# Kernel optimization log

Measured on AMD Instinct MI355X. Metric: run time of the kernel, lower is better.

The kernel has to match this reference:

```python
import jax, jax.numpy as jnp
import numpy as np

IN_DIM = 128
D_MODEL = 2 * IN_DIM        # 256, Mamba d_model
D_INNER = 2 * D_MODEL       # 512, expand=2
D_STATE = 16
D_CONV = 4
DT_RANK = (D_MODEL + 15) // 16  # 16
B = 4
C = 1024                    # original channel dim -> Mamba sequence length
EPS = 1e-5


def rmsnorm(x, w):
    return x * jax.lax.rsqrt(jnp.mean(x * x, axis=-1, keepdims=True) + EPS) * w


def conv1x1(x, w, b):
    # x: (B, Cin, L); 1x1 conv == channel matmul
    return jnp.einsum('oi,bil->bol', w, x) + b[None, :, None]


def mamba(u, in_w, conv_w, conv_b, xproj_w, dt_w, dt_b, A_log, Dp, out_w):
    # u: (B, L, D_MODEL) -- faithful mamba_ssm Mamba block (defaults)
    di, K = conv_w.shape
    n = A_log.shape[1]
    r = dt_w.shape[1]
    xz = u @ in_w.T                              # (B,L,2*di)
    xx, z = jnp.split(xz, 2, axis=-1)
    # depthwise causal conv over L
    xt = jnp.pad(jnp.transpose(xx, (0, 2, 1)), ((0, 0), (0, 0), (K - 1, 0)))
    xc = jax.lax.conv_general_dilated(xt, conv_w[:, None, :], (1,), 'VALID',
                                      feature_group_count=di)
    xx = jax.nn.silu(jnp.transpose(xc + conv_b[None, :, None], (0, 2, 1)))
    dbl = xx @ xproj_w.T                         # (B,L,r+2n)
    dt, Bm, Cm = dbl[..., :r], dbl[..., r:r + n], dbl[..., r + n:]
    dt = jax.nn.softplus(dt @ dt_w.T + dt_b)     # (B,L,di)
    A = -jnp.exp(A_log)                          # (di,n)
    dA = jnp.exp(dt[..., None] * A)              # (B,L,di,n)
    dBx = (dt * xx)[..., None] * Bm[:, :, None, :]

    def step(h, inps):
        dA_t, dBx_t, C_t = inps
        h = dA_t * h + dBx_t
        return h, jnp.einsum('bdn,bn->bd', h, C_t)

    h0 = jnp.zeros((u.shape[0], di, n), u.dtype)
    _, ys = jax.lax.scan(step, h0, (jnp.moveaxis(dA, 1, 0),
                                    jnp.moveaxis(dBx, 1, 0),
                                    jnp.moveaxis(Cm, 1, 0)))
    y = jnp.moveaxis(ys, 0, 1) + xx * Dp
    return (y * jax.nn.silu(z)) @ out_w.T


def postnorm_mamba(u, params, norm_w):
    return rmsnorm(mamba(u, *params), norm_w) + u


def _forward(x, W_in, b_in, W_wp, b_wp, W_fp, b_fp, W_bp, b_bp, W_out, b_out,
             norm_w_top,
             f_in_w, f_conv_w, f_conv_b, f_xproj_w, f_dt_w, f_dt_b, f_A_log, f_D, f_out_w, f_norm_w,
             bk_in_w, bk_conv_w, bk_conv_b, bk_xproj_w, bk_dt_w, bk_dt_b, bk_A_log, bk_D, bk_out_w, bk_norm_w):
    residual = x                                  # (B, C, L)
    xn = rmsnorm(x, norm_w_top)                   # RMSNorm over L
    xt = jnp.transpose(xn, (0, 2, 1))             # (B, L, C); L acts as conv channels
    ssm_in = conv1x1(xt, W_in, b_in)              # (B, 2L, C)
    # forward branch
    fwd = conv1x1(ssm_in, W_fp, b_fp)
    fwd = jnp.transpose(fwd, (0, 2, 1))           # (B, C, 2L): Mamba seq=C
    fwd = postnorm_mamba(fwd, (f_in_w, f_conv_w, f_conv_b, f_xproj_w, f_dt_w,
                               f_dt_b, f_A_log, f_D, f_out_w), f_norm_w)
    fwd = jnp.transpose(fwd, (0, 2, 1))           # (B, 2L, C)
    # backward branch (flip along C)
    bwd = conv1x1(ssm_in[:, :, ::-1], W_bp, b_bp)
    bwd = jnp.transpose(bwd, (0, 2, 1))
    bwd = postnorm_mamba(bwd, (bk_in_w, bk_conv_w, bk_conv_b, bk_xproj_w, bk_dt_w,
                               bk_dt_b, bk_A_log, bk_D, bk_out_w), bk_norm_w)
    bwd = jnp.transpose(bwd, (0, 2, 1))[:, :, ::-1]
    # swish gate
    w = conv1x1(xt, W_wp, b_wp)
    w = w * jax.nn.sigmoid(w)
    out = conv1x1(w * fwd + w * bwd, W_out, b_out)  # (B, L, C)
    return jnp.transpose(out, (0, 2, 1)) + residual  # (B, C, L)


def setup_inputs():
    key = jax.random.key(0)
    ks = iter(jax.random.split(key, 64))
    rn = lambda shape, s=0.02: jax.random.normal(next(ks), shape, jnp.float32) * s
    inp = {"x": jax.random.normal(next(ks), (B, C, IN_DIM), jnp.float32)}
    inp["W_in"] = rn((2 * IN_DIM, IN_DIM));   inp["b_in"] = rn((2 * IN_DIM,), 0.1)
    inp["W_wp"] = rn((2 * IN_DIM, IN_DIM));   inp["b_wp"] = rn((2 * IN_DIM,), 0.1)
    inp["W_fp"] = rn((2 * IN_DIM, 2 * IN_DIM)); inp["b_fp"] = rn((2 * IN_DIM,), 0.1)
    inp["W_bp"] = rn((2 * IN_DIM, 2 * IN_DIM)); inp["b_bp"] = rn((2 * IN_DIM,), 0.1)
    inp["W_out"] = rn((IN_DIM, 2 * IN_DIM));  inp["b_out"] = rn((IN_DIM,), 0.1)
    inp["norm_w_top"] = jnp.ones((IN_DIM,), jnp.float32)
    A_init = jnp.log(jnp.broadcast_to(jnp.arange(1, D_STATE + 1, dtype=jnp.float32),
                                      (D_INNER, D_STATE)))
    for p in ("f", "bk"):
        inp[p + "_in_w"] = rn((2 * D_INNER, D_MODEL))
        inp[p + "_conv_w"] = rn((D_INNER, D_CONV), 0.2)
        inp[p + "_conv_b"] = rn((D_INNER,), 0.1)
        inp[p + "_xproj_w"] = rn((DT_RANK + 2 * D_STATE, D_INNER))
        inp[p + "_dt_w"] = rn((D_INNER, DT_RANK), 0.1)
        inp[p + "_dt_b"] = rn((D_INNER,), 0.5)
        inp[p + "_A_log"] = A_init
        inp[p + "_D"] = jnp.ones((D_INNER,), jnp.float32)
        inp[p + "_out_w"] = rn((D_MODEL, D_INNER))
        inp[p + "_norm_w"] = jnp.ones((D_MODEL,), jnp.float32)
    return inp


def reference(x, W_in, b_in, W_wp, b_wp, W_fp, b_fp, W_bp, b_bp, W_out, b_out,
              norm_w_top,
              f_in_w, f_conv_w, f_conv_b, f_xproj_w, f_dt_w, f_dt_b, f_A_log, f_D, f_out_w, f_norm_w,
              bk_in_w, bk_conv_w, bk_conv_b, bk_xproj_w, bk_dt_w, bk_dt_b, bk_A_log, bk_D, bk_out_w, bk_norm_w):
    return _forward(x, W_in, b_in, W_wp, b_wp, W_fp, b_fp, W_bp, b_bp, W_out, b_out,
                    norm_w_top,
                    f_in_w, f_conv_w, f_conv_b, f_xproj_w, f_dt_w, f_dt_b, f_A_log, f_D, f_out_w, f_norm_w,
                    bk_in_w, bk_conv_w, bk_conv_b, bk_xproj_w, bk_dt_w, bk_dt_b, bk_A_log, bk_D, bk_out_w, bk_norm_w)
```

## Files before the change

kernel.cpp:

```cpp
#include <hip/hip_runtime.h>
#include <math.h>

#define C_LEN 1024
#define NROW 4096
#define NCHUNK 32
#define CHUNK 32

typedef __attribute__((ext_vector_type(8))) short short8;
typedef __attribute__((ext_vector_type(4))) float f32x4;

__device__ __forceinline__ float siluf(float x) { return x / (1.f + __expf(-x)); }

__device__ __forceinline__ unsigned short f2bf(float f) {
    unsigned u = __builtin_bit_cast(unsigned, f);
    unsigned r = (u + 0x7FFFu + ((u >> 16) & 1u)) >> 16;
    return (unsigned short)r;
}
__device__ __forceinline__ float bf2f(unsigned short v) {
    unsigned u = ((unsigned)v) << 16;
    return __builtin_bit_cast(float, u);
}

struct WTab {
    const float* s[6];
    unsigned short* d[6];
    int n[6];
};
__global__ __launch_bounds__(256) void k_prep(WTab t, const float* __restrict__ x,
                                              const float* __restrict__ nw,
                                              unsigned short* __restrict__ xn_bf,
                                              const float* __restrict__ W_fp,
                                              const float* __restrict__ W_bp,
                                              const float* __restrict__ W_in,
                                              const float* __restrict__ b_in,
                                              const float* __restrict__ b_fp,
                                              const float* __restrict__ b_bp,
                                              const float* __restrict__ b_wp,
                                              float* __restrict__ Wpin,
                                              float* __restrict__ bmega,
                                              unsigned short* __restrict__ Wmega) {
    int seg = blockIdx.y;
    if (seg < 6) {
        int n = t.n[seg];
        int i = (blockIdx.x * 256 + threadIdx.x) * 4;
        if (i < n) {
            float4 v = *(const float4*)(t.s[seg] + i);
            unsigned short* o = t.d[seg] + i;
            o[0] = f2bf(v.x); o[1] = f2bf(v.y); o[2] = f2bf(v.z); o[3] = f2bf(v.w);
        }
    } else if (seg == 6) {
        int wave = threadIdx.x >> 6, lane = threadIdx.x & 63;
        #pragma unroll
        for (int it = 0; it < 4; ++it) {
            int row = blockIdx.x * 16 + it * 4 + wave;
            if (row < 4096) {
                float2 v = ((const float2*)(x + (size_t)row * 128))[lane];
                float ss = v.x * v.x + v.y * v.y;
                #pragma unroll
                for (int off = 32; off; off >>= 1) ss += __shfl_xor(ss, off, 64);
                float rs = rsqrtf(ss * (1.f / 128.f) + 1e-5f);
                float2 wv = ((const float2*)nw)[lane];
                ushort2 o;
                o.x = f2bf(v.x * rs * wv.x);
                o.y = f2bf(v.y * rs * wv.y);
                ((ushort2*)(xn_bf + (size_t)row * 128))[lane] = o;
            }
        }
    } else {
        int tg = blockIdx.x * 256 + threadIdx.x;
        if (tg < 65536) {
            int p = tg >> 15, rem = tg & 32767;
            int o = rem >> 7, i = rem & 127;
            const float* Wsrc = p ? W_bp : W_fp;
            float s = 0.f;
            #pragma unroll 8
            for (int j = 0; j < 256; ++j) s += Wsrc[o * 256 + j] * W_in[j * 128 + i];
            Wpin[p * 32768 + o * 128 + i] = s;
            Wmega[(size_t)(p * 256 + o) * 128 + i] = f2bf(s);
        } else if (tg < 66048) {
            int q = tg - 65536;
            int p = q >> 8, o = q & 255;
            const float* Wsrc = p ? W_bp : W_fp;
            const float* badd = p ? b_bp : b_fp;
            float s = badd[o];
            #pragma unroll 8
            for (int j = 0; j < 256; ++j) s += Wsrc[o * 256 + j] * b_in[j];
            bmega[p * 256 + o] = s;
        } else if (tg < 66304) {
            int q = tg - 66048;
            bmega[512 + q] = b_wp[q];
        }
    }
}

__global__ __launch_bounds__(256) void k_wcomb2(const float* __restrict__ f_in_w,
                                                const float* __restrict__ bk_in_w,
                                                const float* __restrict__ Wpin,
                                                unsigned short* __restrict__ Wmega,
                                                float* __restrict__ bmega) {
    int tg = blockIdx.x * 256 + threadIdx.x;
    if (tg < 262144) {
        int p = tg >> 17, rem = tg & 131071;
        int o = rem >> 7, i = rem & 127;
        const float* inw = p ? bk_in_w : f_in_w;
        const float* wp = Wpin + p * 32768;
        float s = 0.f;
        #pragma unroll 8
        for (int j = 0; j < 256; ++j) s += inw[o * 256 + j] * wp[j * 128 + i];
        Wmega[(size_t)(768 + p * 1024 + o) * 128 + i] = f2bf(s);
    } else if (tg < 264192) {
        int q = tg - 262144;
        int p = q >> 10, o = q & 1023;
        const float* inw = p ? bk_in_w : f_in_w;
        const float* bp = bmega + p * 256;
        float s = 0.f;
        #pragma unroll 8
        for (int j = 0; j < 256; ++j) s += inw[o * 256 + j] * bp[j];
        bmega[768 + p * 1024 + o] = s;
    }
}

__global__ __launch_bounds__(256) void k_megagemm(const unsigned short* __restrict__ A,
                                                  const unsigned short* __restrict__ W,
                                                  const float* __restrict__ bias,
                                                  unsigned short* __restrict__ uf,
                                                  unsigned short* __restrict__ ub,
                                                  unsigned short* __restrict__ wbuf,
                                                  unsigned short* __restrict__ xzF,
                                                  unsigned short* __restrict__ xzB) {
    __shared__ __align__(16) unsigned short As[128 * 72];
    __shared__ __align__(16) unsigned short Bs[64 * 72];
    const int K = 128;
    int tid = threadIdx.x;
    int m0 = blockIdx.y * 128, n0 = blockIdx.x * 64;
    int w = tid >> 6, lane = tid & 63;
    int q = lane >> 4, ln = lane & 15;

    unsigned short* Cb; int stride, nc0; bool flip = false, dosilu = false;
    if (n0 < 256)       { Cb = uf;   stride = 256;  nc0 = n0; }
    else if (n0 < 512)  { Cb = ub;   stride = 256;  nc0 = n0 - 256;  flip = true; }
    else if (n0 < 768)  { Cb = wbuf; stride = 256;  nc0 = n0 - 512;  dosilu = true; }
    else if (n0 < 1792) { Cb = xzF;  stride = 1024; nc0 = n0 - 768; }
    else                { Cb = xzB;  stride = 1024; nc0 = n0 - 1792; flip = true; }

    int arow0 = tid >> 1;
    int aseg0 = (tid & 1) * 32;
    int brow = tid >> 2, bseg = (tid & 3) * 16;
    const unsigned short* pa = A + (size_t)(m0 + arow0) * K + aseg0;
    const unsigned short* pw = W + (size_t)(n0 + brow) * K + bseg;

    f32x4 acc[2][4];
    #pragma unroll
    for (int i = 0; i < 2; ++i)
        #pragma unroll
        for (int j = 0; j < 4; ++j) acc[i][j] = (f32x4)(0.f);

    for (int k0 = 0; k0 < K; k0 += 64) {
        #pragma unroll
        for (int h = 0; h < 4; ++h)
            *(short8*)&As[arow0 * 72 + aseg0 + h * 8] = *(const short8*)(pa + h * 8);
        *(short8*)&Bs[brow * 72 + bseg]     = *(const short8*)pw;
        *(short8*)&Bs[brow * 72 + bseg + 8] = *(const short8*)(pw + 8);
        pa += 64; pw += 64;
        __syncthreads();
        short8 a0[2], a1[2];
        #pragma unroll
        for (int i = 0; i < 2; ++i) {
            int row = w * 32 + i * 16 + ln;
            a0[i] = *(const short8*)&As[row * 72 + q * 8];
            a1[i] = *(const short8*)&As[row * 72 + 32 + q * 8];
        }
        #pragma unroll
        for (int j = 0; j < 4; ++j) {
            short8 bf0 = *(const short8*)&Bs[(j * 16 + ln) * 72 + q * 8];
            short8 bf1 = *(const short8*)&Bs[(j * 16 + ln) * 72 + 32 + q * 8];
            #pragma unroll
            for (int i = 0; i < 2; ++i) {
                acc[i][j] = __builtin_amdgcn_mfma_f32_16x16x32_bf16(a0[i], bf0, acc[i][j], 0, 0, 0);
                acc[i][j] = __builtin_amdgcn_mfma_f32_16x16x32_bf16(a1[i], bf1, acc[i][j], 0, 0, 0);
            }
        }
        __syncthreads();
    }
    #pragma unroll
    for (int j = 0; j < 4; ++j) {
        float bsv = bias[n0 + j * 16 + ln];
        int nc = nc0 + j * 16 + ln;
        #pragma unroll
        for (int i = 0; i < 2; ++i) {
            #pragma unroll
            for (int r = 0; r < 4; ++r) {
                int m = m0 + w * 32 + i * 16 + q * 4 + r;
                int mw = flip ? (m ^ (C_LEN - 1)) : m;
                float v = acc[i][j][r] + bsv;
                if (dosilu) v = siluf(v);
                Cb[(size_t)mw * stride + nc] = f2bf(v);
            }
        }
    }
}

__global__ __launch_bounds__(256) void k_gemm128(
        const unsigned short* __restrict__ A0, const unsigned short* __restrict__ A1,
        const unsigned short* __restrict__ W0, const unsigned short* __restrict__ W1,
        unsigned short* __restrict__ Cb0, unsigned short* __restrict__ Cb1,
        int N, int K) {
    __shared__ __align__(16) unsigned short As[128 * 72];
    __shared__ __align__(16) unsigned short Bs[64 * 72];
    int p = blockIdx.z;
    const unsigned short* A = p ? A1 : A0;
    const unsigned short* W = p ? W1 : W0;
    unsigned short* Cbf = p ? Cb1 : Cb0;
    int tid = threadIdx.x;
    int m0 = blockIdx.y * 128, n0 = blockIdx.x * 64;
    int w = tid >> 6, lane = tid & 63;
    int q = lane >> 4, ln = lane & 15;

    int arow0 = tid >> 1;
    int aseg0 = (tid & 1) * 32;
    int brow = tid >> 2, bseg = (tid & 3) * 16;
    const unsigned short* pa = A + (size_t)(m0 + arow0) * K + aseg0;
    const unsigned short* pw = W + (size_t)(n0 + brow) * K + bseg;

    f32x4 acc[2][4];
    #pragma unroll
    for (int i = 0; i < 2; ++i)
        #pragma unroll
        for (int j = 0; j < 4; ++j) acc[i][j] = (f32x4)(0.f);

    for (int k0 = 0; k0 < K; k0 += 64) {
        #pragma unroll
        for (int h = 0; h < 4; ++h)
            *(short8*)&As[arow0 * 72 + aseg0 + h * 8] = *(const short8*)(pa + h * 8);
        *(short8*)&Bs[brow * 72 + bseg]     = *(const short8*)pw;
        *(short8*)&Bs[brow * 72 + bseg + 8] = *(const short8*)(pw + 8);
        pa += 64; pw += 64;
        __syncthreads();
        short8 a0[2], a1[2];
        #pragma unroll
        for (int i = 0; i < 2; ++i) {
            int row = w * 32 + i * 16 + ln;
            a0[i] = *(const short8*)&As[row * 72 + q * 8];
            a1[i] = *(const short8*)&As[row * 72 + 32 + q * 8];
        }
        #pragma unroll
        for (int j = 0; j < 4; ++j) {
            short8 bf0 = *(const short8*)&Bs[(j * 16 + ln) * 72 + q * 8];
            short8 bf1 = *(const short8*)&Bs[(j * 16 + ln) * 72 + 32 + q * 8];
            #pragma unroll
            for (int i = 0; i < 2; ++i) {
                acc[i][j] = __builtin_amdgcn_mfma_f32_16x16x32_bf16(a0[i], bf0, acc[i][j], 0, 0, 0);
                acc[i][j] = __builtin_amdgcn_mfma_f32_16x16x32_bf16(a1[i], bf1, acc[i][j], 0, 0, 0);
            }
        }
        __syncthreads();
    }
    #pragma unroll
    for (int i = 0; i < 2; ++i)
        #pragma unroll
        for (int j = 0; j < 4; ++j) {
            int nn = n0 + j * 16 + ln;
            #pragma unroll
            for (int r = 0; r < 4; ++r) {
                int m = m0 + w * 32 + i * 16 + q * 4 + r;
                Cbf[(size_t)m * N + nn] = f2bf(acc[i][j][r]);
            }
        }
}

__global__ __launch_bounds__(256) void k_gemm2f(
        const unsigned short* __restrict__ A0, const unsigned short* __restrict__ A1,
        const unsigned short* __restrict__ W0, const unsigned short* __restrict__ W1,
        float* __restrict__ Cf0, float* __restrict__ Cf1,
        int N, int K) {
    __shared__ __align__(16) unsigned short As[64 * 72];
    __shared__ __align__(16) unsigned short Bs[64 * 72];
    int p = blockIdx.z;
    const unsigned short* A = p ? A1 : A0;
    const unsigned short* W = p ? W1 : W0;
    float* Cf = p ? Cf1 : Cf0;
    int tid = threadIdx.x;
    int m0 = blockIdx.y * 64, n0 = blockIdx.x * 64;
    int w = tid >> 6, lane = tid & 63;
    int q = lane >> 4, ln = lane & 15;
    int srow = tid >> 2;
    int sseg = (tid & 3) * 16;

    const unsigned short* pa = A + (size_t)(m0 + srow) * K + sseg;
    int nIdx = n0 + srow;
    const unsigned short* pw = W + (size_t)nIdx * K + sseg;
    bool nOK = (nIdx < N);

    f32x4 acc[4];
    #pragma unroll
    for (int j = 0; j < 4; ++j) acc[j] = (f32x4)(0.f);

    for (int k0 = 0; k0 < K; k0 += 64) {
        *(short8*)&As[srow * 72 + sseg]     = *(const short8*)pa;
        *(short8*)&As[srow * 72 + sseg + 8] = *(const short8*)(pa + 8);
        short8 b0 = (short8)(0), b1 = (short8)(0);
        if (nOK) { b0 = *(const short8*)pw; b1 = *(const short8*)(pw + 8); }
        *(short8*)&Bs[srow * 72 + sseg] = b0;
        *(short8*)&Bs[srow * 72 + sseg + 8] = b1;
        pa += 64; pw += 64;
        __syncthreads();
        short8 af0 = *(const short8*)&As[(w * 16 + ln) * 72 + q * 8];
        short8 af1 = *(const short8*)&As[(w * 16 + ln) * 72 + 32 + q * 8];
        #pragma unroll
        for (int j = 0; j < 4; ++j) {
            short8 bf0 = *(const short8*)&Bs[(j * 16 + ln) * 72 + q * 8];
            short8 bf1 = *(const short8*)&Bs[(j * 16 + ln) * 72 + 32 + q * 8];
            acc[j] = __builtin_amdgcn_mfma_f32_16x16x32_bf16(af0, bf0, acc[j], 0, 0, 0);
            acc[j] = __builtin_amdgcn_mfma_f32_16x16x32_bf16(af1, bf1, acc[j], 0, 0, 0);
        }
        __syncthreads();
    }
    #pragma unroll
    for (int j = 0; j < 4; ++j) {
        int nn = n0 + j * 16 + ln;
        if (nn < N) {
            #pragma unroll
            for (int r = 0; r < 4; ++r) {
                int m = m0 + w * 16 + q * 4 + r;
                Cf[(size_t)m * N + nn] = acc[j][r];
            }
        }
    }
}

__global__ __launch_bounds__(256) void k_gemm_out(const unsigned short* __restrict__ A,
                                                  const unsigned short* __restrict__ W,
                                                  const float* __restrict__ bias,
                                                  const float* __restrict__ resid,
                                                  float* __restrict__ Cf) {
    __shared__ __align__(16) unsigned short As[64 * 72];
    __shared__ __align__(16) unsigned short Bs[64 * 72];
    const int N = 128, K = 256;
    int tid = threadIdx.x;
    int m0 = blockIdx.y * 64, n0 = blockIdx.x * 64;
    int w = tid >> 6, lane = tid & 63;
    int q = lane >> 4, ln = lane & 15;
    int srow = tid >> 2;
    int sseg = (tid & 3) * 16;

    const unsigned short* pa = A + (size_t)(m0 + srow) * K + sseg;
    const unsigned short* pw = W + (size_t)(n0 + srow) * K + sseg;

    f32x4 acc[4];
    #pragma unroll
    for (int j = 0; j < 4; ++j) acc[j] = (f32x4)(0.f);

    for (int k0 = 0; k0 < K; k0 += 64) {
        *(short8*)&As[srow * 72 + sseg]     = *(const short8*)pa;
        *(short8*)&As[srow * 72 + sseg + 8] = *(const short8*)(pa + 8);
        *(short8*)&Bs[srow * 72 + sseg]     = *(const short8*)pw;
        *(short8*)&Bs[srow * 72 + sseg + 8] = *(const short8*)(pw + 8);
        pa += 64; pw += 64;
        __syncthreads();
        short8 af0 = *(const short8*)&As[(w * 16 + ln) * 72 + q * 8];
        short8 af1 = *(const short8*)&As[(w * 16 + ln) * 72 + 32 + q * 8];
        #pragma unroll
        for (int j = 0; j < 4; ++j) {
            short8 bf0 = *(const short8*)&Bs[(j * 16 + ln) * 72 + q * 8];
            short8 bf1 = *(const short8*)&Bs[(j * 16 + ln) * 72 + 32 + q * 8];
            acc[j] = __builtin_amdgcn_mfma_f32_16x16x32_bf16(af0, bf0, acc[j], 0, 0, 0);
            acc[j] = __builtin_amdgcn_mfma_f32_16x16x32_bf16(af1, bf1, acc[j], 0, 0, 0);
        }
        __syncthreads();
    }
    #pragma unroll
    for (int j = 0; j < 4; ++j) {
        int nn = n0 + j * 16 + ln;
        float bsv = bias[nn];
        #pragma unroll
        for (int r = 0; r < 4; ++r) {
            int m = m0 + w * 16 + q * 4 + r;
            Cf[(size_t)m * N + nn] = acc[j][r] + bsv + resid[(size_t)m * N + nn];
        }
    }
}

__global__ __launch_bounds__(256) void k_conv(const unsigned short* __restrict__ xz0,
                                              const unsigned short* __restrict__ xz1,
                                              const float* __restrict__ cw0,
                                              const float* __restrict__ cw1,
                                              const float* __restrict__ cb0,
                                              const float* __restrict__ cb1,
                                              unsigned short* __restrict__ xc0,
                                              unsigned short* __restrict__ xc1) {
    int pz = blockIdx.z;
    const unsigned short* xz = pz ? xz1 : xz0;
    const float* cw = pz ? cw1 : cw0;
    const float* cb = pz ? cb1 : cb0;
    unsigned short* xconv_bf = pz ? xc1 : xc0;
    int d = blockIdx.x * 256 + threadIdx.x;
    int by = blockIdx.y;
    int b = by >> 6, c0 = (by & 63) * 16;
    float4 cwv = *(const float4*)(cw + d * 4);
    float bias = cb[d];
    const unsigned short* base = xz + (size_t)(b * C_LEN) * 1024 + d;
    float w0 = 0.f, w1 = 0.f, w2 = 0.f;
    if (c0) {
        w0 = bf2f(base[(size_t)(c0 - 3) * 1024]);
        w1 = bf2f(base[(size_t)(c0 - 2) * 1024]);
        w2 = bf2f(base[(size_t)(c0 - 1) * 1024]);
    }
    unsigned short* out = xconv_bf + (size_t)(b * C_LEN + c0) * 512 + d;
    #pragma unroll
    for (int i = 0; i < 16; ++i) {
        float cur = bf2f(base[(size_t)(c0 + i) * 1024]);
        float acc = bias;
        acc = fmaf(cwv.x, w0, acc);
        acc = fmaf(cwv.y, w1, acc);
        acc = fmaf(cwv.z, w2, acc);
        acc = fmaf(cwv.w, cur, acc);
        out[(size_t)i * 512] = f2bf(siluf(acc));
        w0 = w1; w1 = w2; w2 = cur;
    }
}

__global__ __launch_bounds__(256) void k_dtproj(const float* __restrict__ dbl0,
                                                const float* __restrict__ dbl1,
                                                const float* __restrict__ dtw0,
                                                const float* __restrict__ dtw1,
                                                const float* __restrict__ dtb0,
                                                const float* __restrict__ dtb1,
                                                unsigned short* __restrict__ dt0,
                                                unsigned short* __restrict__ dt1) {
    int pz = blockIdx.z;
    const float* dbl = pz ? dbl1 : dbl0;
    const float* dtw = pz ? dtw1 : dtw0;
    const float* dtb = pz ? dtb1 : dtb0;
    unsigned short* dt = pz ? dt1 : dt0;
    int d = blockIdx.x * 256 + threadIdx.x;
    int r0 = blockIdx.y * 8;
    float4 w0 = *(const float4*)(dtw + d * 16);
    float4 w1 = *(const float4*)(dtw + d * 16 + 4);
    float4 w2 = *(const float4*)(dtw + d * 16 + 8);
    float4 w3 = *(const float4*)(dtw + d * 16 + 12);
    float bias = dtb[d];
    #pragma unroll
    for (int rr = 0; rr < 8; ++rr) {
        int r = r0 + rr;
        const float* row = dbl + (size_t)r * 48;
        float s = bias;
        s = fmaf(row[0], w0.x, s);  s = fmaf(row[1], w0.y, s);
        s = fmaf(row[2], w0.z, s);  s = fmaf(row[3], w0.w, s);
        s = fmaf(row[4], w1.x, s);  s = fmaf(row[5], w1.y, s);
        s = fmaf(row[6], w1.z, s);  s = fmaf(row[7], w1.w, s);
        s = fmaf(row[8], w2.x, s);  s = fmaf(row[9], w2.y, s);
        s = fmaf(row[10], w2.z, s); s = fmaf(row[11], w2.w, s);
        s = fmaf(row[12], w3.x, s); s = fmaf(row[13], w3.y, s);
        s = fmaf(row[14], w3.z, s); s = fmaf(row[15], w3.w, s);
        float sp = fmaxf(s, 0.f) + log1pf(__expf(-fabsf(s)));
        dt[(size_t)r * 512 + d] = f2bf(sp);
    }
}

__global__ __launch_bounds__(256) void k_scan1(const unsigned short* __restrict__ dt0,
                                               const unsigned short* __restrict__ dt1,
                                               const unsigned short* __restrict__ xc0,
                                               const unsigned short* __restrict__ xc1,
                                               const float* __restrict__ dblA,
                                               const float* __restrict__ dblB,
                                               const float* __restrict__ alog0,
                                               const float* __restrict__ alog1,
                                               float* __restrict__ hfin0,
                                               float* __restrict__ hfin1,
                                               float* __restrict__ Pfin0,
                                               float* __restrict__ Pfin1) {
    int z = blockIdx.z;
    int b = z & 3, p = z >> 2;
    const unsigned short* dt = p ? dt1 : dt0;
    const unsigned short* xconv_bf = p ? xc1 : xc0;
    const float* dbl = p ? dblB : dblA;
    const float* A_log = p ? alog1 : alog0;
    float* hfin = p ? hfin1 : hfin0;
    float* Pfin = p ? Pfin1 : Pfin0;
    int tid = threadIdx.x;
    int nh = tid & 1, dl = tid >> 1;
    int k = blockIdx.x, dg = blockIdx.y;
    int d = dg * 128 + dl;
    float4 al0 = *(const float4*)&A_log[d * 16 + nh * 8];
    float4 al1 = *(const float4*)&A_log[d * 16 + nh * 8 + 4];
    float Ac[8] = {-__expf(al0.x), -__expf(al0.y), -__expf(al0.z), -__expf(al0.w),
                   -__expf(al1.x), -__expf(al1.y), -__expf(al1.z), -__expf(al1.w)};
    size_t r0 = (size_t)(b * C_LEN + k * CHUNK);
    const unsigned short* pdt = dt + r0 * 512 + d;
    const unsigned short* pxv = xconv_bf + r0 * 512 + d;
    const float* pB  = dbl + r0 * 48 + 16 + nh * 8;
    float h[8] = {0.f, 0.f, 0.f, 0.f, 0.f, 0.f, 0.f, 0.f};
    float sdt = 0.f;
    #pragma unroll 8
    for (int c = 0; c < CHUNK; ++c) {
        float dtv = bf2f(*pdt);
        float xv  = bf2f(*pxv);
        float4 B0 = *(const float4*)pB;
        float4 B1 = *(const float4*)(pB + 4);
        float dx = dtv * xv;
        float Bv[8] = {B0.x, B0.y, B0.z, B0.w, B1.x, B1.y, B1.z, B1.w};
        #pragma unroll
        for (int j = 0; j < 8; ++j)
            h[j] = fmaf(__expf(dtv * Ac[j]), h[j], dx * Bv[j]);
        sdt += dtv;
        pdt += 512; pxv += 512; pB += 48;
    }
    size_t idx = ((size_t)(b * NCHUNK + k) * 512 + d) * 16 + nh * 8;
    *(float4*)&hfin[idx]     = make_float4(h[0], h[1], h[2], h[3]);
    *(float4*)&hfin[idx + 4] = make_float4(h[4], h[5], h[6], h[7]);
    *(float4*)&Pfin[idx]     = make_float4(__expf(Ac[0] * sdt), __expf(Ac[1] * sdt),
                                           __expf(Ac[2] * sdt), __expf(Ac[3] * sdt));
    *(float4*)&Pfin[idx + 4] = make_float4(__expf(Ac[4] * sdt), __expf(Ac[5] * sdt),
                                           __expf(Ac[6] * sdt), __expf(Ac[7] * sdt));
}

__global__ __launch_bounds__(256) void k_scan2(const float* __restrict__ hfin0,
                                               const float* __restrict__ hfin1,
                                               float* __restrict__ Pfin0,
                                               float* __restrict__ Pfin1) {
    int tt = blockIdx.x * 256 + threadIdx.x;
    int p = tt >> 15;
    int t = tt & 32767;
    const float* hfin = p ? hfin1 : hfin0;
    float* Pfin = p ? Pfin1 : Pfin0;
    int b = t >> 13;
    int dn = t & 8191;
    float carry = 0.f;
    #pragma unroll
    for (int k = 0; k < NCHUNK; ++k) {
        size_t idx = (size_t)(b * NCHUNK + k) * 8192 + dn;
        float pv = Pfin[idx];
        float hf = hfin[idx];
        Pfin[idx] = carry;
        carry = fmaf(pv, carry, hf);
    }
}

__global__ __launch_bounds__(256) void k_scan3(const unsigned short* __restrict__ dt0,
                                               const unsigned short* __restrict__ dt1,
                                               const unsigned short* __restrict__ xc0,
                                               const unsigned short* __restrict__ xc1,
                                               const float* __restrict__ dblA,
                                               const float* __restrict__ dblB,
                                               const unsigned short* __restrict__ xz0,
                                               const unsigned short* __restrict__ xz1,
                                               const float* __restrict__ alog0,
                                               const float* __restrict__ alog1,
                                               const float* __restrict__ Dp0,
                                               const float* __restrict__ Dp1,
                                               const float* __restrict__ carry0,
                                               const float* __restrict__ carry1,
                                               unsigned short* __restrict__ g0,
                                               unsigned short* __restrict__ g1) {
    int z = blockIdx.z;
    int b = z & 3, p = z >> 2;
    const unsigned short* dt = p ? dt1 : dt0;
    const unsigned short* xconv_bf = p ? xc1 : xc0;
    const float* dbl = p ? dblB : dblA;
    const unsigned short* xz = p ? xz1 : xz0;
    const float* A_log = p ? alog1 : alog0;
    const float* Dp = p ? Dp1 : Dp0;
    const float* carryArr = p ? carry1 : carry0;
    unsigned short* gated_bf = p ? g1 : g0;
    int tid = threadIdx.x;
    int nh = tid & 1, dl = tid >> 1;
    int k = blockIdx.x, dg = blockIdx.y;
    int d = dg * 128 + dl;
    float4 al0 = *(const float4*)&A_log[d * 16 + nh * 8];
    float4 al1 = *(const float4*)&A_log[d * 16 + nh * 8 + 4];
    float Ac[8] = {-__expf(al0.x), -__expf(al0.y), -__expf(al0.z), -__expf(al0.w),
                   -__expf(al1.x), -__expf(al1.y), -__expf(al1.z), -__expf(al1.w)};
    float Dd = Dp[d];
    size_t idx = ((size_t)(b * NCHUNK + k) * 512 + d) * 16 + nh * 8;
    float4 h0 = *(const float4*)&carryArr[idx];
    float4 h1 = *(const float4*)&carryArr[idx + 4];
    float h[8] = {h0.x, h0.y, h0.z, h0.w, h1.x, h1.y, h1.z, h1.w};
    size_t r0 = (size_t)(b * C_LEN + k * CHUNK);
    const unsigned short* pdt = dt + r0 * 512 + d;
    const unsigned short* pxv = xconv_bf + r0 * 512 + d;
    const float* pB  = dbl + r0 * 48 + 16 + nh * 8;
    const float* pC  = dbl + r0 * 48 + 32 + nh * 8;
    const unsigned short* pz = xz + r0 * 1024 + 512 + d;
    unsigned short* pg = gated_bf + r0 * 512 + d;
    #pragma unroll 4
    for (int c = 0; c < CHUNK; ++c) {
        float dtv = bf2f(*pdt);
        float xv  = bf2f(*pxv);
        float4 B0 = *(const float4*)pB;
        float4 B1 = *(const float4*)(pB + 4);
        float4 C0 = *(const float4*)pC;
        float4 C1 = *(const float4*)(pC + 4);
        float dx = dtv * xv;
        float Bv[8] = {B0.x, B0.y, B0.z, B0.w, B1.x, B1.y, B1.z, B1.w};
        float Cv[8] = {C0.x, C0.y, C0.z, C0.w, C1.x, C1.y, C1.z, C1.w};
        float contrib = 0.f;
        #pragma unroll
        for (int j = 0; j < 8; ++j) {
            h[j] = fmaf(__expf(dtv * Ac[j]), h[j], dx * Bv[j]);
            contrib = fmaf(h[j], Cv[j], contrib);
        }
        contrib += __shfl_xor(contrib, 1, 64);
        if (nh == 0) {
            float y = contrib + xv * Dd;
            float zv = bf2f(*pz);
            *pg = f2bf(y * siluf(zv));
        }
        pdt += 512; pxv += 512; pB += 48; pC += 48; pz += 1024; pg += 512;
    }
}

__global__ __launch_bounds__(256) void k_postcomb(const unsigned short* __restrict__ mo0,
                                                  const unsigned short* __restrict__ mo1,
                                                  const float* __restrict__ w0,
                                                  const float* __restrict__ w1,
                                                  const unsigned short* __restrict__ uf,
                                                  const unsigned short* __restrict__ ub,
                                                  const unsigned short* __restrict__ wbuf,
                                                  unsigned short* __restrict__ Acomb) {
    __shared__ float red[8];
    int r = blockIdx.x, t = threadIdx.x;
    int rf = r ^ (C_LEN - 1);
    float v0 = bf2f(mo0[(size_t)r * 256 + t]);
    float v1 = bf2f(mo1[(size_t)rf * 256 + t]);
    float ss0 = v0 * v0, ss1 = v1 * v1;
    #pragma unroll
    for (int off = 32; off; off >>= 1) {
        ss0 += __shfl_xor(ss0, off, 64);
        ss1 += __shfl_xor(ss1, off, 64);
    }
    if ((t & 63) == 0) { red[t >> 6] = ss0; red[4 + (t >> 6)] = ss1; }
    __syncthreads();
    float rs0 = rsqrtf((red[0] + red[1] + red[2] + red[3]) * (1.f / 256.f) + 1e-5f);
    float rs1 = rsqrtf((red[4] + red[5] + red[6] + red[7]) * (1.f / 256.f) + 1e-5f);
    float mofv = v0 * rs0 * w0[t] + bf2f(uf[(size_t)r * 256 + t]);
    float mobv = v1 * rs1 * w1[t] + bf2f(ub[(size_t)rf * 256 + t]);
    Acomb[(size_t)r * 256 + t] = f2bf(bf2f(wbuf[(size_t)r * 256 + t]) * (mofv + mobv));
}

extern "C" void kernel_launch(void* const* d_in, const int* in_sizes, int n_in,
                              void* d_out, int out_size, void* d_ws, size_t ws_size,
                              hipStream_t stream) {
    const float* x          = (const float*)d_in[0];
    const float* W_in       = (const float*)d_in[1];
    const float* b_in       = (const float*)d_in[2];
    const float* W_wp       = (const float*)d_in[3];
    const float* b_wp       = (const float*)d_in[4];
    const float* W_fp       = (const float*)d_in[5];
    const float* b_fp       = (const float*)d_in[6];
    const float* W_bp       = (const float*)d_in[7];
    const float* b_bp       = (const float*)d_in[8];
    const float* W_out      = (const float*)d_in[9];
    const float* b_out      = (const float*)d_in[10];
    const float* norm_w_top = (const float*)d_in[11];
    const float* mamba_p[2][10];
    for (int p = 0; p < 2; ++p)
        for (int i = 0; i < 10; ++i)
            mamba_p[p][i] = (const float*)d_in[12 + p * 10 + i];

    float* ws = (float*)d_ws;
    float* dblP[2]  = {ws + 0,       ws + 196608};
    unsigned short* dtsP[2] = {(unsigned short*)(ws + 393216),
                               (unsigned short*)(ws + 2490368)};
    float* Wpin  = ws + 1441792;
    float* bmega = ws + 1507328;
    float* hfinP[2] = {ws + 4587520, ws + 5636096};
    float* PfinP[2] = {ws + 6684672, ws + 7733248};

    unsigned short* us = (unsigned short*)(ws + 8781824);
    unsigned short* xn_bf   = us + 0;
    unsigned short* Acomb   = us + 524288;
    unsigned short* uf_bf   = us + 1572864;
    unsigned short* ub_bf   = us + 2621440;
    unsigned short* wbuf_bf = us + 3670016;
    unsigned short* xzP[2]  = {us + 4718592,  us + 8912896};
    unsigned short* xcP[2]  = {us + 13107200, us + 15204352};
    unsigned short* gP[2]   = {us + 17301504, us + 19398656};
    unsigned short* moP[2]  = {us + 21495808, us + 22544384};
    unsigned short* Wmega   = us + 23592960;
    unsigned short* wb      = us + 25690112;
    unsigned short* wb_W_out = wb + 196608;
    unsigned short* wb_xp[2]  = {wb + 491520, wb + 909312};
    unsigned short* wb_outw[2]= {wb + 516096, wb + 933888};

    WTab t;
    t.s[0] = W_wp;            t.d[0] = Wmega + 512 * 128; t.n[0] = 32768;
    t.s[1] = W_out;           t.d[1] = wb_W_out;          t.n[1] = 32768;
    t.s[2] = mamba_p[0][3];   t.d[2] = wb_xp[0];          t.n[2] = 24576;
    t.s[3] = mamba_p[0][8];   t.d[3] = wb_outw[0];        t.n[3] = 131072;
    t.s[4] = mamba_p[1][3];   t.d[4] = wb_xp[1];          t.n[4] = 24576;
    t.s[5] = mamba_p[1][8];   t.d[5] = wb_outw[1];        t.n[5] = 131072;
    k_prep<<<dim3(260, 8), 256, 0, stream>>>(t, x, norm_w_top, xn_bf,
                                             W_fp, W_bp, W_in, b_in, b_fp, b_bp, b_wp,
                                             Wpin, bmega, Wmega);
    k_wcomb2<<<1040, 256, 0, stream>>>(mamba_p[0][0], mamba_p[1][0], Wpin, Wmega, bmega);
    k_megagemm<<<dim3(44, 32), 256, 0, stream>>>(xn_bf, Wmega, bmega,
                                                 uf_bf, ub_bf, wbuf_bf, xzP[0], xzP[1]);
    k_conv<<<dim3(2, 256, 2), 256, 0, stream>>>(xzP[0], xzP[1],
                                                mamba_p[0][1], mamba_p[1][1],
                                                mamba_p[0][2], mamba_p[1][2],
                                                xcP[0], xcP[1]);
    k_gemm2f<<<dim3(1, 64, 2), 256, 0, stream>>>(xcP[0], xcP[1], wb_xp[0], wb_xp[1],
                                                 dblP[0], dblP[1], 48, 512);
    k_dtproj<<<dim3(2, 512, 2), 256, 0, stream>>>(dblP[0], dblP[1],
                                                  mamba_p[0][4], mamba_p[1][4],
                                                  mamba_p[0][5], mamba_p[1][5],
                                                  dtsP[0], dtsP[1]);
    k_scan1<<<dim3(NCHUNK, 4, 8), 256, 0, stream>>>(dtsP[0], dtsP[1], xcP[0], xcP[1],
                                                    dblP[0], dblP[1],
                                                    mamba_p[0][6], mamba_p[1][6],
                                                    hfinP[0], hfinP[1], PfinP[0], PfinP[1]);
    k_scan2<<<256, 256, 0, stream>>>(hfinP[0], hfinP[1], PfinP[0], PfinP[1]);
    k_scan3<<<dim3(NCHUNK, 4, 8), 256, 0, stream>>>(dtsP[0], dtsP[1], xcP[0], xcP[1],
                                                    dblP[0], dblP[1], xzP[0], xzP[1],
                                                    mamba_p[0][6], mamba_p[1][6],
                                                    mamba_p[0][7], mamba_p[1][7],
                                                    PfinP[0], PfinP[1], gP[0], gP[1]);
    k_gemm128<<<dim3(4, 32, 2), 256, 0, stream>>>(gP[0], gP[1], wb_outw[0], wb_outw[1],
                                                  moP[0], moP[1], 256, 512);
    k_postcomb<<<NROW, 256, 0, stream>>>(moP[0], moP[1],
                                         mamba_p[0][9], mamba_p[1][9],
                                         uf_bf, ub_bf, wbuf_bf, Acomb);
    k_gemm_out<<<dim3(2, 64), 256, 0, stream>>>(Acomb, wb_W_out, b_out, x, (float*)d_out);
}
```

Before: 278.3 us.

## Fuse conv, x-projection and dt-projection; fuse post-norm combine into output GEMM

New measurement: 372.9 us. 34.0% more time.

```diff
diff --git a/kernel.cpp b/kernel.cpp
--- a/kernel.cpp
+++ b/kernel.cpp
@@ -268,44 +268,87 @@
         }
 }
 
-__global__ __launch_bounds__(256) void k_gemm2f(
-        const unsigned short* __restrict__ A0, const unsigned short* __restrict__ A1,
+__global__ __launch_bounds__(256) void k_convdbl(
+        const unsigned short* __restrict__ xz0, const unsigned short* __restrict__ xz1,
+        const float* __restrict__ cw0, const float* __restrict__ cw1,
+        const float* __restrict__ cb0, const float* __restrict__ cb1,
         const unsigned short* __restrict__ W0, const unsigned short* __restrict__ W1,
+        const float* __restrict__ dtw0, const float* __restrict__ dtw1,
+        const float* __restrict__ dtb0, const float* __restrict__ dtb1,
+        unsigned short* __restrict__ xcO0, unsigned short* __restrict__ xcO1,
         float* __restrict__ Cf0, float* __restrict__ Cf1,
-        int N, int K) {
-    __shared__ __align__(16) unsigned short As[64 * 72];
+        unsigned short* __restrict__ dtO0, unsigned short* __restrict__ dtO1) {
+    __shared__ __align__(16) unsigned short As64[64 * 520];
     __shared__ __align__(16) unsigned short Bs[64 * 72];
-    int p = blockIdx.z;
-    const unsigned short* A = p ? A1 : A0;
+    __shared__ float dblS[64][17];
+    const int N = 48, K = 512;
+    int p = blockIdx.y;
+    const unsigned short* xz = p ? xz1 : xz0;
+    const float* cw = p ? cw1 : cw0;
+    const float* cb = p ? cb1 : cb0;
     const unsigned short* W = p ? W1 : W0;
+    const float* dtw = p ? dtw1 : dtw0;
+    const float* dtb = p ? dtb1 : dtb0;
+    unsigned short* xcO = p ? xcO1 : xcO0;
     float* Cf = p ? Cf1 : Cf0;
+    unsigned short* dtO = p ? dtO1 : dtO0;
+
     int tid = threadIdx.x;
-    int m0 = blockIdx.y * 64, n0 = blockIdx.x * 64;
+    int m0 = blockIdx.x * 64;
+    int bstart = m0 & ~(C_LEN - 1);
+
+    {
+        int d0 = tid * 2;
+        float4 cwa = *(const float4*)(cw + d0 * 4);
+        float4 cwb = *(const float4*)(cw + d0 * 4 + 4);
+        float cba = cb[d0], cbb = cb[d0 + 1];
+        float a0 = 0.f, a1 = 0.f, a2 = 0.f;
+        float b0 = 0.f, b1 = 0.f, b2 = 0.f;
+        for (int r = m0 - 3; r < m0 + 64; ++r) {
+            float ca = 0.f, cbv = 0.f;
+            if (r >= bstart) {
+                unsigned u = *(const unsigned*)(xz + (size_t)r * 1024 + d0);
+                ca  = bf2f((unsigned short)(u & 0xFFFFu));
+                cbv = bf2f((unsigned short)(u >> 16));
+            }
+            if (r >= m0) {
+                float sa = cba, sb = cbb;
+                sa = fmaf(cwa.x, a0, sa); sa = fmaf(cwa.y, a1, sa);
+                sa = fmaf(cwa.z, a2, sa); sa = fmaf(cwa.w, ca, sa);
+                sb = fmaf(cwb.x, b0, sb); sb = fmaf(cwb.y, b1, sb);
+                sb = fmaf(cwb.z, b2, sb); sb = fmaf(cwb.w, cbv, sb);
+                unsigned short oa = f2bf(siluf(sa));
+                unsigned short ob = f2bf(siluf(sb));
+                unsigned pack = (unsigned)oa | ((unsigned)ob << 16);
+                *(unsigned*)&As64[(r - m0) * 520 + d0] = pack;
+                *(unsigned*)(xcO + (size_t)r * 512 + d0) = pack;
+            }
+            a0 = a1; a1 = a2; a2 = ca;
+            b0 = b1; b1 = b2; b2 = cbv;
+        }
+    }
+    __syncthreads();
+
     int w = tid >> 6, lane = tid & 63;
     int q = lane >> 4, ln = lane & 15;
     int srow = tid >> 2;
     int sseg = (tid & 3) * 16;
-
-    const unsigned short* pa = A + (size_t)(m0 + srow) * K + sseg;
-    int nIdx = n0 + srow;
-    const unsigned short* pw = W + (size_t)nIdx * K + sseg;
-    bool nOK = (nIdx < N);
+    const unsigned short* pw = W + (size_t)srow * K + sseg;
+    bool nOK = (srow < N);
 
     f32x4 acc[4];
     #pragma unroll
     for (int j = 0; j < 4; ++j) acc[j] = (f32x4)(0.f);
 
     for (int k0 = 0; k0 < K; k0 += 64) {
-        *(short8*)&As[srow * 72 + sseg]     = *(const short8*)pa;
-        *(short8*)&As[srow * 72 + sseg + 8] = *(const short8*)(pa + 8);
-        short8 b0 = (short8)(0), b1 = (short8)(0);
-        if (nOK) { b0 = *(const short8*)pw; b1 = *(const short8*)(pw + 8); }
-        *(short8*)&Bs[srow * 72 + sseg] = b0;
-        *(short8*)&Bs[srow * 72 + sseg + 8] = b1;
-        pa += 64; pw += 64;
+        short8 bb0 = (short8)(0), bb1 = (short8)(0);
+        if (nOK) { bb0 = *(const short8*)pw; bb1 = *(const short8*)(pw + 8); }
+        *(short8*)&Bs[srow * 72 + sseg] = bb0;
+        *(short8*)&Bs[srow * 72 + sseg + 8] = bb1;
+        pw += 64;
         __syncthreads();
-        short8 af0 = *(const short8*)&As[(w * 16 + ln) * 72 + q * 8];
-        short8 af1 = *(const short8*)&As[(w * 16 + ln) * 72 + 32 + q * 8];
+        short8 af0 = *(const short8*)&As64[(w * 16 + ln) * 520 + k0 + q * 8];
+        short8 af1 = *(const short8*)&As64[(w * 16 + ln) * 520 + k0 + 32 + q * 8];
         #pragma unroll
         for (int j = 0; j < 4; ++j) {
             short8 bf0 = *(const short8*)&Bs[(j * 16 + ln) * 72 + q * 8];
@@ -317,143 +360,36 @@
     }
     #pragma unroll
     for (int j = 0; j < 4; ++j) {
-        int nn = n0 + j * 16 + ln;
-        if (nn < N) {
-            #pragma unroll
-            for (int r = 0; r < 4; ++r) {
-                int m = m0 + w * 16 + q * 4 + r;
-                Cf[(size_t)m * N + nn] = acc[j][r];
-            }
-        }
-    }
-}
-
-__global__ __launch_bounds__(256) void k_gemm_out(const unsigned short* __restrict__ A,
-                                                  const unsigned short* __restrict__ W,
-                                                  const float* __restrict__ bias,
-                                                  const float* __restrict__ resid,
-                                                  float* __restrict__ Cf) {
-    __shared__ __align__(16) unsigned short As[64 * 72];
-    __shared__ __align__(16) unsigned short Bs[64 * 72];
-    const int N = 128, K = 256;
-    int tid = threadIdx.x;
-    int m0 = blockIdx.y * 64, n0 = blockIdx.x * 64;
-    int w = tid >> 6, lane = tid & 63;
-    int q = lane >> 4, ln = lane & 15;
-    int srow = tid >> 2;
-    int sseg = (tid & 3) * 16;
-
-    const unsigned short* pa = A + (size_t)(m0 + srow) * K + sseg;
-    const unsigned short* pw = W + (size_t)(n0 + srow) * K + sseg;
-
-    f32x4 acc[4];
-    #pragma unroll
-    for (int j = 0; j < 4; ++j) acc[j] = (f32x4)(0.f);
-
-    for (int k0 = 0; k0 < K; k0 += 64) {
-        *(short8*)&As[srow * 72 + sseg]     = *(const short8*)pa;
-        *(short8*)&As[srow * 72 + sseg + 8] = *(const short8*)(pa + 8);
-        *(short8*)&Bs[srow * 72 + sseg]     = *(const short8*)pw;
-        *(short8*)&Bs[srow * 72 + sseg + 8] = *(const short8*)(pw + 8);
-        pa += 64; pw += 64;
-        __syncthreads();
-        short8 af0 = *(const short8*)&As[(w * 16 + ln) * 72 + q * 8];
-        short8 af1 = *(const short8*)&As[(w * 16 + ln) * 72 + 32 + q * 8];
-        #pragma unroll
-        for (int j = 0; j < 4; ++j) {
-            short8 bf0 = *(const short8*)&Bs[(j * 16 + ln) * 72 + q * 8];
-            short8 bf1 = *(const short8*)&Bs[(j * 16 + ln) * 72 + 32 + q * 8];
-            acc[j] = __builtin_amdgcn_mfma_f32_16x16x32_bf16(af0, bf0, acc[j], 0, 0, 0);
-            acc[j] = __builtin_amdgcn_mfma_f32_16x16x32_bf16(af1, bf1, acc[j], 0, 0, 0);
-        }
-        __syncthreads();
-    }
-    #pragma unroll
-    for (int j = 0; j < 4; ++j) {
-        int nn = n0 + j * 16 + ln;
-        float bsv = bias[nn];
+        int nn = j * 16 + ln;
         #pragma unroll
         for (int r = 0; r < 4; ++r) {
-            int m = m0 + w * 16 + q * 4 + r;
-            Cf[(size_t)m * N + nn] = acc[j][r] + bsv + resid[(size_t)m * N + nn];
-        }
-    }
-}
-
-__global__ __launch_bounds__(256) void k_conv(const unsigned short* __restrict__ xz0,
-                                              const unsigned short* __restrict__ xz1,
-                                              const float* __restrict__ cw0,
-                                              const float* __restrict__ cw1,
-                                              const float* __restrict__ cb0,
-                                              const float* __restrict__ cb1,
-                                              unsigned short* __restrict__ xc0,
-                                              unsigned short* __restrict__ xc1) {
-    int pz = blockIdx.z;
-    const unsigned short* xz = pz ? xz1 : xz0;
-    const float* cw = pz ? cw1 : cw0;
-    const float* cb = pz ? cb1 : cb0;
-    unsigned short* xconv_bf = pz ? xc1 : xc0;
-    int d = blockIdx.x * 256 + threadIdx.x;
-    int by = blockIdx.y;
-    int b = by >> 6, c0 = (by & 63) * 16;
-    float4 cwv = *(const float4*)(cw + d * 4);
-    float bias = cb[d];
-    const unsigned short* base = xz + (size_t)(b * C_LEN) * 1024 + d;
-    float w0 = 0.f, w1 = 0.f, w2 = 0.f;
-    if (c0) {
-        w0 = bf2f(base[(size_t)(c0 - 3) * 1024]);
-        w1 = bf2f(base[(size_t)(c0 - 2) * 1024]);
-        w2 = bf2f(base[(size_t)(c0 - 1) * 1024]);
-    }
-    unsigned short* out = xconv_bf + (size_t)(b * C_LEN + c0) * 512 + d;
-    #pragma unroll
-    for (int i = 0; i < 16; ++i) {
-        float cur = bf2f(base[(size_t)(c0 + i) * 1024]);
-        float acc = bias;
-        acc = fmaf(cwv.x, w0, acc);
-        acc = fmaf(cwv.y, w1, acc);
-        acc = fmaf(cwv.z, w2, acc);
-        acc = fmaf(cwv.w, cur, acc);
-        out[(size_t)i * 512] = f2bf(siluf(acc));
-        w0 = w1; w1 = w2; w2 = cur;
-    }
-}
-
-__global__ __launch_bounds__(256) void k_dtproj(const float* __restrict__ dbl0,
-                                                const float* __restrict__ dbl1,
-                                                const float* __restrict__ dtw0,
-                                                const float* __restrict__ dtw1,
-                                                const float* __restrict__ dtb0,
-                                                const float* __restrict__ dtb1,
-                                                unsigned short* __restrict__ dt0,
-                                                unsigned short* __restrict__ dt1) {
-    int pz = blockIdx.z;
-    const float* dbl = pz ? dbl1 : dbl0;
-    const float* dtw = pz ? dtw1 : dtw0;
-    const float* dtb = pz ? dtb1 : dtb0;
-    unsigned short* dt = pz ? dt1 : dt0;
-    int d = blockIdx.x * 256 + threadIdx.x;
-    int r0 = blockIdx.y * 8;
-    float4 w0 = *(const float4*)(dtw + d * 16);
-    float4 w1 = *(const float4*)(dtw + d * 16 + 4);
-    float4 w2 = *(const float4*)(dtw + d * 16 + 8);
-    float4 w3 = *(const float4*)(dtw + d * 16 + 12);
-    float bias = dtb[d];
-    #pragma unroll
-    for (int rr = 0; rr < 8; ++rr) {
-        int r = r0 + rr;
-        const float* row = dbl + (size_t)r * 48;
-        float s = bias;
-        s = fmaf(row[0], w0.x, s);  s = fmaf(row[1], w0.y, s);
-        s = fmaf(row[2], w0.z, s);  s = fmaf(row[3], w0.w, s);
-        s = fmaf(row[4], w1.x, s);  s = fmaf(row[5], w1.y, s);
-        s = fmaf(row[6], w1.z, s);  s = fmaf(row[7], w1.w, s);
-        s = fmaf(row[8], w2.x, s);  s = fmaf(row[9], w2.y, s);
-        s = fmaf(row[10], w2.z, s); s = fmaf(row[11], w2.w, s);
-        s = fmaf(row[12], w3.x, s); s = fmaf(row[13], w3.y, s);
-        s = fmaf(row[14], w3.z, s); s = fmaf(row[15], w3.w, s);
+            int mloc = w * 16 + q * 4 + r;
+            if (nn < N) Cf[(size_t)(m0 + mloc) * N + nn] = acc[j][r];
+            if (j == 0 && ln < 16) dblS[mloc][ln] = acc[0][r];
+        }
+    }
+    __syncthreads();
+    int row = tid >> 2, dseg = tid & 3;
+    float rv[16];
+    #pragma unroll
+    for (int kk = 0; kk < 16; ++kk) rv[kk] = dblS[row][kk];
+    unsigned short* dto = dtO + (size_t)(m0 + row) * 512 + dseg * 128;
+    const float* dtwb = dtw + (size_t)dseg * 128 * 16;
+    for (int dd = 0; dd < 128; ++dd) {
+        const float4* wr = (const float4*)(dtwb + dd * 16);
+        float biasv = dtb[dseg * 128 + dd];
+        float4 w0v = wr[0], w1v = wr[1], w2v = wr[2], w3v = wr[3];
+        float s = biasv;
+        s = fmaf(rv[0], w0v.x, s);  s = fmaf(rv[1], w0v.y, s);
+        s = fmaf(rv[2], w0v.z, s);  s = fmaf(rv[3], w0v.w, s);
+        s = fmaf(rv[4], w1v.x, s);  s = fmaf(rv[5], w1v.y, s);
+        s = fmaf(rv[6], w1v.z, s);  s = fmaf(rv[7], w1v.w, s);
+        s = fmaf(rv[8], w2v.x, s);  s = fmaf(rv[9], w2v.y, s);
+        s = fmaf(rv[10], w2v.z, s); s = fmaf(rv[11], w2v.w, s);
+        s = fmaf(rv[12], w3v.x, s); s = fmaf(rv[13], w3v.y, s);
+        s = fmaf(rv[14], w3v.z, s); s = fmaf(rv[15], w3v.w, s);
         float sp = fmaxf(s, 0.f) + log1pf(__expf(-fabsf(s)));
-        dt[(size_t)r * 512 + d] = f2bf(sp);
+        dto[dd] = f2bf(sp);
     }
 }
 
@@ -609,32 +545,111 @@
     }
 }
 
-__global__ __launch_bounds__(256) void k_postcomb(const unsigned short* __restrict__ mo0,
-                                                  const unsigned short* __restrict__ mo1,
-                                                  const float* __restrict__ w0,
-                                                  const float* __restrict__ w1,
-                                                  const unsigned short* __restrict__ uf,
-                                                  const unsigned short* __restrict__ ub,
-                                                  const unsigned short* __restrict__ wbuf,
-                                                  unsigned short* __restrict__ Acomb) {
-    __shared__ float red[8];
-    int r = blockIdx.x, t = threadIdx.x;
-    int rf = r ^ (C_LEN - 1);
-    float v0 = bf2f(mo0[(size_t)r * 256 + t]);
-    float v1 = bf2f(mo1[(size_t)rf * 256 + t]);
-    float ss0 = v0 * v0, ss1 = v1 * v1;
-    #pragma unroll
-    for (int off = 32; off; off >>= 1) {
-        ss0 += __shfl_xor(ss0, off, 64);
-        ss1 += __shfl_xor(ss1, off, 64);
-    }
-    if ((t & 63) == 0) { red[t >> 6] = ss0; red[4 + (t >> 6)] = ss1; }
+__global__ __launch_bounds__(256) void k_outcomb(
+        const unsigned short* __restrict__ mo0, const unsigned short* __restrict__ mo1,
+        const float* __restrict__ nw0, const float* __restrict__ nw1,
+        const unsigned short* __restrict__ uf, const unsigned short* __restrict__ ub,
+        const unsigned short* __restrict__ wbuf,
+        const unsigned short* __restrict__ W,
+        const float* __restrict__ bias,
+        const float* __restrict__ resid,
+        float* __restrict__ Cf) {
+    __shared__ __align__(16) unsigned short As[64 * 264];
+    __shared__ __align__(16) unsigned short Bs[128 * 72];
+    const int K = 256;
+    int tid = threadIdx.x;
+    int m0 = blockIdx.x * 64;
+
+    {
+        int row = tid >> 2, qq = tid & 3;
+        int r = m0 + row;
+        int rf = r ^ (C_LEN - 1);
+        int c0 = qq * 64;
+        const unsigned short* pm0 = mo0 + (size_t)r * 256 + c0;
+        const unsigned short* pm1 = mo1 + (size_t)rf * 256 + c0;
+        float ss0 = 0.f, ss1 = 0.f;
+        #pragma unroll
+        for (int c = 0; c < 64; c += 8) {
+            short8 v0 = *(const short8*)(pm0 + c);
+            short8 v1 = *(const short8*)(pm1 + c);
+            #pragma unroll
+            for (int j = 0; j < 8; ++j) {
+                float f0 = bf2f((unsigned short)v0[j]);
+                float f1 = bf2f((unsigned short)v1[j]);
+                ss0 = fmaf(f0, f0, ss0);
+                ss1 = fmaf(f1, f1, ss1);
+            }
+        }
+        ss0 += __shfl_xor(ss0, 1, 64); ss0 += __shfl_xor(ss0, 2, 64);
+        ss1 += __shfl_xor(ss1, 1, 64); ss1 += __shfl_xor(ss1, 2, 64);
+        float rs0 = rsqrtf(ss0 * (1.f / 256.f) + 1e-5f);
+        float rs1 = rsqrtf(ss1 * (1.f / 256.f) + 1e-5f);
+        const unsigned short* pu = uf + (size_t)r * 256 + c0;
+        const unsigned short* pb = ub + (size_t)rf * 256 + c0;
+        const unsigned short* pwv = wbuf + (size_t)r * 256 + c0;
+        #pragma unroll
+        for (int c = 0; c < 64; c += 8) {
+            short8 v0 = *(const short8*)(pm0 + c);
+            short8 v1 = *(const short8*)(pm1 + c);
+            short8 vu = *(const short8*)(pu + c);
+            short8 vb = *(const short8*)(pb + c);
+            short8 vw = *(const short8*)(pwv + c);
+            float4 wa0 = *(const float4*)(nw0 + c0 + c);
+            float4 wa1 = *(const float4*)(nw0 + c0 + c + 4);
+            float4 wb0 = *(const float4*)(nw1 + c0 + c);
+            float4 wb1 = *(const float4*)(nw1 + c0 + c + 4);
+            float wav[8] = {wa0.x, wa0.y, wa0.z, wa0.w, wa1.x, wa1.y, wa1.z, wa1.w};
+            float wbv[8] = {wb0.x, wb0.y, wb0.z, wb0.w, wb1.x, wb1.y, wb1.z, wb1.w};
+            short8 o;
+            #pragma unroll
+            for (int j = 0; j < 8; ++j) {
+                float mf = bf2f((unsigned short)v0[j]) * rs0 * wav[j] +
+                           bf2f((unsigned short)vu[j]);
+                float mb = bf2f((unsigned short)v1[j]) * rs1 * wbv[j] +
+                           bf2f((unsigned short)vb[j]);
+                o[j] = (short)f2bf(bf2f((unsigned short)vw[j]) * (mf + mb));
+            }
+            *(short8*)&As[row * 264 + c0 + c] = o;
+        }
+    }
     __syncthreads();
-    float rs0 = rsqrtf((red[0] + red[1] + red[2] + red[3]) * (1.f / 256.f) + 1e-5f);
-    float rs1 = rsqrtf((red[4] + red[5] + red[6] + red[7]) * (1.f / 256.f) + 1e-5f);
-    float mofv = v0 * rs0 * w0[t] + bf2f(uf[(size_t)r * 256 + t]);
-    float mobv = v1 * rs1 * w1[t] + bf2f(ub[(size_t)rf * 256 + t]);
-    Acomb[(size_t)r * 256 + t] = f2bf(bf2f(wbuf[(size_t)r * 256 + t]) * (mofv + mobv));
+
+    int w = tid >> 6, lane = tid & 63;
+    int q = lane >> 4, ln = lane & 15;
+    int brow = tid >> 1, bseg = (tid & 1) * 32;
+    const unsigned short* pw = W + (size_t)brow * K + bseg;
+
+    f32x4 acc[8];
+    #pragma unroll
+    for (int j = 0; j < 8; ++j) acc[j] = (f32x4)(0.f);
+
+    for (int k0 = 0; k0 < K; k0 += 64) {
+        #pragma unroll
+        for (int h = 0; h < 4; ++h)
+            *(short8*)&Bs[brow * 72 + bseg + h * 8] = *(const short8*)(pw + h * 8);
+        pw += 64;
+        __syncthreads();
+        short8 af0 = *(const short8*)&As[(w * 16 + ln) * 264 + k0 + q * 8];
+        short8 af1 = *(const short8*)&As[(w * 16 + ln) * 264 + k0 + 32 + q * 8];
+        #pragma unroll
+        for (int j = 0; j < 8; ++j) {
+            short8 bf0 = *(const short8*)&Bs[(j * 16 + ln) * 72 + q * 8];
+            short8 bf1 = *(const short8*)&Bs[(j * 16 + ln) * 72 + 32 + q * 8];
+            acc[j] = __builtin_amdgcn_mfma_f32_16x16x32_bf16(af0, bf0, acc[j], 0, 0, 0);
+            acc[j] = __builtin_amdgcn_mfma_f32_16x16x32_bf16(af1, bf1, acc[j], 0, 0, 0);
+        }
+        __syncthreads();
+    }
+    #pragma unroll
+    for (int j = 0; j < 8; ++j) {
+        int nn = j * 16 + ln;
+        float bsv = bias[nn];
+        #pragma unroll
+        for (int r = 0; r < 4; ++r) {
+            int m = m0 + w * 16 + q * 4 + r;
+            Cf[(size_t)m * 128 + nn] = acc[j][r] + bsv + resid[(size_t)m * 128 + nn];
+        }
+    }
 }
 
 extern "C" void kernel_launch(void* const* d_in, const int* in_sizes, int n_in,
@@ -668,7 +683,6 @@
 
     unsigned short* us = (unsigned short*)(ws + 8781824);
     unsigned short* xn_bf   = us + 0;
-    unsigned short* Acomb   = us + 524288;
     unsigned short* uf_bf   = us + 1572864;
     unsigned short* ub_bf   = us + 2621440;
     unsigned short* wbuf_bf = us + 3670016;
@@ -695,16 +709,15 @@
     k_wcomb2<<<1040, 256, 0, stream>>>(mamba_p[0][0], mamba_p[1][0], Wpin, Wmega, bmega);
     k_megagemm<<<dim3(44, 32), 256, 0, stream>>>(xn_bf, Wmega, bmega,
                                                  uf_bf, ub_bf, wbuf_bf, xzP[0], xzP[1]);
-    k_conv<<<dim3(2, 256, 2), 256, 0, stream>>>(xzP[0], xzP[1],
-                                                mamba_p[0][1], mamba_p[1][1],
-                                                mamba_p[0][2], mamba_p[1][2],
-                                                xcP[0], xcP[1]);
-    k_gemm2f<<<dim3(1, 64, 2), 256, 0, stream>>>(xcP[0], xcP[1], wb_xp[0], wb_xp[1],
-                                                 dblP[0], dblP[1], 48, 512);
-    k_dtproj<<<dim3(2, 512, 2), 256, 0, stream>>>(dblP[0], dblP[1],
-                                                  mamba_p[0][4], mamba_p[1][4],
-                                                  mamba_p[0][5], mamba_p[1][5],
-                                                  dtsP[0], dtsP[1]);
+    k_convdbl<<<dim3(64, 2), 256, 0, stream>>>(xzP[0], xzP[1],
+                                               mamba_p[0][1], mamba_p[1][1],
+                                               mamba_p[0][2], mamba_p[1][2],
+                                               wb_xp[0], wb_xp[1],
+                                               mamba_p[0][4], mamba_p[1][4],
+                                               mamba_p[0][5], mamba_p[1][5],
+                                               xcP[0], xcP[1],
+                                               dblP[0], dblP[1],
+                                               dtsP[0], dtsP[1]);
     k_scan1<<<dim3(NCHUNK, 4, 8), 256, 0, stream>>>(dtsP[0], dtsP[1], xcP[0], xcP[1],
                                                     dblP[0], dblP[1],
                                                     mamba_p[0][6], mamba_p[1][6],
@@ -717,8 +730,8 @@
                                                     PfinP[0], PfinP[1], gP[0], gP[1]);
     k_gemm128<<<dim3(4, 32, 2), 256, 0, stream>>>(gP[0], gP[1], wb_outw[0], wb_outw[1],
                                                   moP[0], moP[1], 256, 512);
-    k_postcomb<<<NROW, 256, 0, stream>>>(moP[0], moP[1],
-                                         mamba_p[0][9], mamba_p[1][9],
-                                         uf_bf, ub_bf, wbuf_bf, Acomb);
-    k_gemm_out<<<dim3(2, 64), 256, 0, stream>>>(Acomb, wb_W_out, b_out, x, (float*)d_out);
-}
+    k_outcomb<<<64, 256, 0, stream>>>(moP[0], moP[1],
+                                      mamba_p[0][9], mamba_p[1][9],
+                                      uf_bf, ub_bf, wbuf_bf,
+                                      wb_W_out, b_out, x, (float*)d_out);
+}
```
